# Kernel optimization log

Hardware: AMD Instinct MI355X
Metric: run time of the kernel (lower is better)

Reference implementation:

```python
import jax, jax.numpy as jnp
import numpy as np

D_MODEL = 1024
NUM_HEADS = 16
HEAD_DIM = D_MODEL // NUM_HEADS


def setup_inputs() -> dict:
    key = jax.random.key(0)
    ks = jax.random.split(key, 9)
    B, T = 2, 2048
    s = 1.0 / np.sqrt(D_MODEL)
    return {
        "x": jax.random.normal(ks[0], (B, T, D_MODEL), dtype=jnp.float32),
        "Wq": jax.random.normal(ks[1], (D_MODEL, D_MODEL), dtype=jnp.float32) * s,
        "bq": jnp.zeros((D_MODEL,), dtype=jnp.float32),
        "Wk": jax.random.normal(ks[2], (D_MODEL, D_MODEL), dtype=jnp.float32) * s,
        "bk": jnp.zeros((D_MODEL,), dtype=jnp.float32),
        "Wv": jax.random.normal(ks[3], (D_MODEL, D_MODEL), dtype=jnp.float32) * s,
        "bv": jnp.zeros((D_MODEL,), dtype=jnp.float32),
        "Wo": jax.random.normal(ks[4], (D_MODEL, D_MODEL), dtype=jnp.float32) * s,
        "bo": jnp.zeros((D_MODEL,), dtype=jnp.float32),
    }


def reference(x, Wq, bq, Wk, bk, Wv, bv, Wo, bo):
    B, T, D = x.shape
    H, Hd = NUM_HEADS, HEAD_DIM
    # Linear projections; weights stored as [in, out] (torch Linear transposed)
    q = (x @ Wq + bq).reshape(B, T, H, Hd)
    k = (x @ Wk + bk).reshape(B, T, H, Hd)
    v = (x @ Wv + bv).reshape(B, T, H, Hd)
    scale = 1.0 / jnp.sqrt(jnp.asarray(Hd, dtype=x.dtype))
    scores = jnp.einsum("bqhd,bkhd->bhqk", q, k) * scale  # [B,H,T,T]
    attn = jax.nn.softmax(scores, axis=-1)
    ctx = jnp.einsum("bhqk,bkhd->bqhd", attn, v).reshape(B, T, D)
    return ctx @ Wo + bo
```

## Files before the change

### kernel.cpp

```cpp
#include <hip/hip_runtime.h>


typedef unsigned short ushort_t;
typedef __attribute__((ext_vector_type(8))) short bf16x8;
typedef __attribute__((ext_vector_type(4))) short bf16x4;
typedef __attribute__((ext_vector_type(4))) float f32x4;

#define BATCH 2
#define SEQ   2048
#define DM    1024
#define NH    16
#define HD    64
#define MTOT  (BATCH*SEQ)

#if __has_builtin(__builtin_amdgcn_exp2f)
#define EXP2(x) __builtin_amdgcn_exp2f(x)
#else
#define EXP2(x) exp2f(x)
#endif

__device__ __forceinline__ ushort_t f2bf(float f) {
    union { float f; unsigned int u; } v; v.f = f;
    unsigned int r = v.u + 0x7fffu + ((v.u >> 16) & 1u);
    return (ushort_t)(r >> 16);
}

__device__ __forceinline__ void gload_lds16(const void* g, void* l) {
    __builtin_amdgcn_global_load_lds(
        (const __attribute__((address_space(1))) unsigned int*)g,
        (__attribute__((address_space(3))) unsigned int*)l, 16, 0, 0);
}

__global__ __launch_bounds__(256) void prep_kernel(const float* __restrict__ x,
                                                   const float* __restrict__ W0,
                                                   const float* __restrict__ W1,
                                                   const float* __restrict__ W2,
                                                   const float* __restrict__ W3,
                                                   ushort_t* __restrict__ xb,
                                                   ushort_t* __restrict__ Wtb) {
    __shared__ ushort_t tile[64][72];
    int bid = blockIdx.x, tid = threadIdx.x;
    if (bid < 4096) {
        int i = bid * 256 + tid;
        float4 v = ((const float4*)x)[i];
        ushort4 o;
        o.x = f2bf(v.x); o.y = f2bf(v.y); o.z = f2bf(v.z); o.w = f2bf(v.w);
        ((ushort4*)xb)[i] = o;
        return;
    }
    int b2 = bid - 4096;
    const float* Ws[4] = {W0, W1, W2, W3};
    const float* W = Ws[b2 >> 8];
    ushort_t* Wt = Wtb + (size_t)(b2 >> 8) * DM * DM;
    int k0 = ((b2 >> 4) & 15) * 64, n0 = (b2 & 15) * 64;
    int tr = tid >> 4;
    int tc = (tid & 15) * 4;
#pragma unroll
    for (int j = 0; j < 4; j++) {
        int r = j * 16 + tr;
        float4 v = *(const float4*)&W[(size_t)(k0 + r) * DM + n0 + tc];
        tile[r][tc + 0] = f2bf(v.x); tile[r][tc + 1] = f2bf(v.y);
        tile[r][tc + 2] = f2bf(v.z); tile[r][tc + 3] = f2bf(v.w);
    }
    __syncthreads();
#pragma unroll
    for (int j = 0; j < 4; j++) {
        int n = j * 16 + tr;
        ushort4 o;
        o.x = tile[tc + 0][n]; o.y = tile[tc + 1][n];
        o.z = tile[tc + 2][n]; o.w = tile[tc + 3][n];
        *(ushort4*)&Wt[(size_t)(n0 + n) * DM + k0 + tc] = o;
    }
}

__global__ __launch_bounds__(256) void gemm_qkv(const ushort_t* __restrict__ A,
                                                const ushort_t* __restrict__ Wtb,
                                                const float* __restrict__ bq,
                                                const float* __restrict__ bk,
                                                const float* __restrict__ bv,
                                                ushort_t* __restrict__ qo,
                                                ushort_t* __restrict__ ko,
                                                ushort_t* __restrict__ vo) {
    __shared__ ushort_t As[3][128 * 32];
    __shared__ ushort_t Bs[3][128 * 32];
    int sel = blockIdx.x >> 3;
    const ushort_t* Wt = Wtb + (size_t)sel * DM * DM;
    const float* bias = sel == 0 ? bq : (sel == 1 ? bk : bv);
    int tid = threadIdx.x;
    int w = tid >> 6, lane = tid & 63, lr = lane & 15, lg = lane >> 4;
    int wr = w >> 1, wc = w & 1;
    int m0 = blockIdx.y * 128, n0 = (blockIdx.x & 7) * 128;

    int srow = (w * 2) * 16 + (lane >> 2);
    int scb = (lane & 3) * 8;
    const ushort_t* ag = &A[(size_t)(m0 + srow) * DM + scb];
    const ushort_t* bg = &Wt[(size_t)(n0 + srow) * DM + scb];
    int ldst = (w * 2) * 1024;

    f32x4 acc[4][4] = {};

#pragma unroll
    for (int p = 0; p < 2; p++) {
        gload_lds16(ag + (size_t)p * 16 * DM, (char*)As[0] + ldst + p * 1024);
        gload_lds16(bg + (size_t)p * 16 * DM, (char*)Bs[0] + ldst + p * 1024);
    }

    int cur = 0;
    for (int kt = 0; kt < 32; ++kt) {
        if (kt + 1 < 32) {
            int nxt = cur + 1 == 3 ? 0 : cur + 1;
            int k0 = (kt + 1) << 5;
#pragma unroll
            for (int p = 0; p < 2; p++) {
                gload_lds16(ag + (size_t)p * 16 * DM + k0, (char*)As[nxt] + ldst + p * 1024);
                gload_lds16(bg + (size_t)p * 16 * DM + k0, (char*)Bs[nxt] + ldst + p * 1024);
            }
            __builtin_amdgcn_sched_barrier(0);
            asm volatile("s_waitcnt vmcnt(4)" ::: "memory");
        } else {
            __builtin_amdgcn_sched_barrier(0);
            asm volatile("s_waitcnt vmcnt(0)" ::: "memory");
        }
        __builtin_amdgcn_s_barrier();
        __builtin_amdgcn_sched_barrier(0);

        bf16x8 af[4], bfr[4];
#pragma unroll
        for (int i = 0; i < 4; i++) {
            af[i]  = *(const bf16x8*)&As[cur][(wr * 64 + i * 16 + lr) * 32 + lg * 8];
            bfr[i] = *(const bf16x8*)&Bs[cur][(wc * 64 + i * 16 + lr) * 32 + lg * 8];
        }
#pragma unroll
        for (int mi = 0; mi < 4; mi++)
#pragma unroll
            for (int ni = 0; ni < 4; ni++)
                acc[mi][ni] = __builtin_amdgcn_mfma_f32_16x16x32_bf16(
                    af[mi], bfr[ni], acc[mi][ni], 0, 0, 0);
        cur = cur + 1 == 3 ? 0 : cur + 1;
    }

    float scale = (sel == 0) ? 0.125f * 1.44269504f : 1.0f;
#pragma unroll
    for (int mi = 0; mi < 4; mi++) {
#pragma unroll
        for (int ni = 0; ni < 4; ni++) {
            f32x4 a = acc[mi][ni];
            int n = n0 + wc * 64 + ni * 16 + lr;
            float bs = bias[n];
            int mbase = m0 + wr * 64 + mi * 16 + lg * 4;
            int hh = n >> 6, d = n & 63;
            if (sel == 2) {
                int b = mbase >> 11, tt = mbase & 2047;
                size_t base = ((size_t)(b * NH + hh) * HD + d) * SEQ + tt;
                ushort4 pk;
                pk.x = f2bf(a[0] + bs); pk.y = f2bf(a[1] + bs);
                pk.z = f2bf(a[2] + bs); pk.w = f2bf(a[3] + bs);
                *(ushort4*)&vo[base] = pk;
            } else {
                ushort_t* o = sel ? ko : qo;
#pragma unroll
                for (int r = 0; r < 4; r++) {
                    int m = mbase + r;
                    int b = m >> 11, tt = m & 2047;
                    o[((size_t)(b * NH + hh) * SEQ + tt) * HD + d] =
                        f2bf((a[r] + bs) * scale);
                }
            }
        }
    }
}

__global__ __launch_bounds__(256) void gemm_out(const ushort_t* __restrict__ A,
                                                const ushort_t* __restrict__ Wt,
                                                const float* __restrict__ bias,
                                                float* __restrict__ out) {
    __shared__ ushort_t As[3][128 * 32];
    __shared__ ushort_t Bs[3][128 * 32];
    int tid = threadIdx.x;
    int w = tid >> 6, lane = tid & 63, lr = lane & 15, lg = lane >> 4;
    int wr = w >> 1, wc = w & 1;
    int m0 = blockIdx.y * 128, n0 = blockIdx.x * 128;

    int srow = (w * 2) * 16 + (lane >> 2);
    int scb = (lane & 3) * 8;
    const ushort_t* ag = &A[(size_t)(m0 + srow) * DM + scb];
    const ushort_t* bg = &Wt[(size_t)(n0 + srow) * DM + scb];
    int ldst = (w * 2) * 1024;

    f32x4 acc[4][4] = {};

#pragma unroll
    for (int p = 0; p < 2; p++) {
        gload_lds16(ag + (size_t)p * 16 * DM, (char*)As[0] + ldst + p * 1024);
        gload_lds16(bg + (size_t)p * 16 * DM, (char*)Bs[0] + ldst + p * 1024);
    }

    int cur = 0;
    for (int kt = 0; kt < 32; ++kt) {
        if (kt + 1 < 32) {
            int nxt = cur + 1 == 3 ? 0 : cur + 1;
            int k0 = (kt + 1) << 5;
#pragma unroll
            for (int p = 0; p < 2; p++) {
                gload_lds16(ag + (size_t)p * 16 * DM + k0, (char*)As[nxt] + ldst + p * 1024);
                gload_lds16(bg + (size_t)p * 16 * DM + k0, (char*)Bs[nxt] + ldst + p * 1024);
            }
            __builtin_amdgcn_sched_barrier(0);
            asm volatile("s_waitcnt vmcnt(4)" ::: "memory");
        } else {
            __builtin_amdgcn_sched_barrier(0);
            asm volatile("s_waitcnt vmcnt(0)" ::: "memory");
        }
        __builtin_amdgcn_s_barrier();
        __builtin_amdgcn_sched_barrier(0);

        bf16x8 af[4], bfr[4];
#pragma unroll
        for (int i = 0; i < 4; i++) {
            af[i]  = *(const bf16x8*)&As[cur][(wr * 64 + i * 16 + lr) * 32 + lg * 8];
            bfr[i] = *(const bf16x8*)&Bs[cur][(wc * 64 + i * 16 + lr) * 32 + lg * 8];
        }
#pragma unroll
        for (int mi = 0; mi < 4; mi++)
#pragma unroll
            for (int ni = 0; ni < 4; ni++)
                acc[mi][ni] = __builtin_amdgcn_mfma_f32_16x16x32_bf16(
                    af[mi], bfr[ni], acc[mi][ni], 0, 0, 0);
        cur = cur + 1 == 3 ? 0 : cur + 1;
    }

#pragma unroll
    for (int mi = 0; mi < 4; mi++) {
#pragma unroll
        for (int ni = 0; ni < 4; ni++) {
            f32x4 a = acc[mi][ni];
            int n = n0 + wc * 64 + ni * 16 + lr;
            float bs = bias[n];
            int mbase = m0 + wr * 64 + mi * 16 + lg * 4;
#pragma unroll
            for (int r = 0; r < 4; r++)
                out[(size_t)(mbase + r) * DM + n] = a[r] + bs;
        }
    }
}

__device__ __forceinline__ void softmax_pack(f32x4 (&s)[8], float& l_run,
                                             int4 (&pwv)[4]) {
    float rs0 = 0.f, rs1 = 0.f, rs2 = 0.f, rs3 = 0.f;
#pragma unroll
    for (int nt = 0; nt < 8; ++nt) {
        float p0 = EXP2(s[nt][0]);
        float p1 = EXP2(s[nt][1]);
        float p2 = EXP2(s[nt][2]);
        float p3 = EXP2(s[nt][3]);
        s[nt][0] = p0; s[nt][1] = p1; s[nt][2] = p2; s[nt][3] = p3;
        rs0 += p0; rs1 += p1; rs2 += p2; rs3 += p3;
    }
    float rs = (rs0 + rs1) + (rs2 + rs3);
    rs += __shfl_xor(rs, 16);
    rs += __shfl_xor(rs, 32);
    l_run += rs;
#pragma unroll
    for (int kk = 0; kk < 4; ++kk) {
        unsigned pw[4];
#pragma unroll
        for (int hh = 0; hh < 2; ++hh)
#pragma unroll
            for (int pr = 0; pr < 2; ++pr) {
                unsigned rr;
                asm("v_cvt_pk_bf16_f32 %0, %1, %2"
                    : "=v"(rr)
                    : "v"(s[kk + 4 * hh][2 * pr]), "v"(s[kk + 4 * hh][2 * pr + 1]));
                pw[hh * 2 + pr] = rr;
            }
        pwv[kk] = make_int4(pw[0], pw[1], pw[2], pw[3]);
    }
}

__global__ __launch_bounds__(512, 2) void attn_kernel(const ushort_t* __restrict__ Q,
                                                      const ushort_t* __restrict__ Kb,
                                                      const ushort_t* __restrict__ Vt,
                                                      ushort_t* __restrict__ Ctx) {
    __shared__ ushort_t Ks[2][128 * 64];
    __shared__ ushort_t Vs[2][64 * 128];

    int tid = threadIdx.x, w = tid >> 6, lane = tid & 63, lr = lane & 15, lg = lane >> 4;
    int orig = blockIdx.x;
    int wg = (orig & 7) * 32 + (orig >> 3);
    int qb = wg & 7, bh = wg >> 3;
    int q0 = qb * 256;

    const ushort_t* Qp = Q + (size_t)bh * SEQ * HD;
    const ushort_t* Kp = Kb + (size_t)bh * SEQ * HD;
    const ushort_t* Vp = Vt + (size_t)bh * HD * SEQ;

    int qrow = q0 + w * 16 + lr;
    bf16x8 aqA[2], aqB[2];
    aqA[0] = *(const bf16x8*)&Qp[(size_t)qrow * HD + lg * 8];
    aqA[1] = *(const bf16x8*)&Qp[(size_t)qrow * HD + 32 + lg * 8];
    aqB[0] = *(const bf16x8*)&Qp[(size_t)(qrow + 128) * HD + lg * 8];
    aqB[1] = *(const bf16x8*)&Qp[(size_t)(qrow + 128) * HD + 32 + lg * 8];

    f32x4 oaccA[4] = {}, oaccB[4] = {};
    float lA = 0.f, lB = 0.f;

    int krow = tid >> 3, kch = tid & 7;
    int kbyte = krow * 128 + ((kch * 16) ^ ((krow & 7) << 4));
    const ushort_t* kg0 = &Kp[(size_t)krow * HD + kch * 8];
    const ushort_t* kg1 = &Kp[(size_t)(krow + 64) * HD + kch * 8];
    int vrow = tid >> 4, vch = tid & 15;
    int S_a2 = (((vch >> 1) & 3) * 32 + (vch & 1) * 16 + (vch >> 3) * 4) * 2;
    int vswz = (vrow & 7) << 4;
    int vbyte0 = vrow * 256 + (S_a2 ^ vswz);
    int vbyte1 = vrow * 256 + ((S_a2 + 16) ^ vswz);
    const ushort_t* vg0 = &Vp[(size_t)vrow * SEQ + vch * 8];
    const ushort_t* vg1 = &Vp[(size_t)(vrow + 32) * SEQ + vch * 8];

    {
        bf16x8 k0v = *(const bf16x8*)kg0;
        bf16x8 k1v = *(const bf16x8*)kg1;
        bf16x8 v0v = *(const bf16x8*)vg0;
        bf16x8 v1v = *(const bf16x8*)vg1;
        *(bf16x8*)((char*)Ks[0] + kbyte) = k0v;
        *(bf16x8*)((char*)Ks[0] + kbyte + 64 * 128) = k1v;
        union { bf16x8 v; bf16x4 h[2]; } u0, u1;
        u0.v = v0v; u1.v = v1v;
        *(bf16x4*)((char*)Vs[0] + vbyte0) = u0.h[0];
        *(bf16x4*)((char*)Vs[0] + vbyte1) = u0.h[1];
        *(bf16x4*)((char*)Vs[0] + vbyte0 + 32 * 256) = u1.h[0];
        *(bf16x4*)((char*)Vs[0] + vbyte1 + 32 * 256) = u1.h[1];
    }
    __syncthreads();

    int kread = lr * 128;
    int kswz = (lr & 7) << 4;

    for (int t = 0; t < SEQ / 128; ++t) {
        int cur = t & 1;
        bf16x8 kr0, kr1, vr0, vr1;
        bool more = (t + 1 < SEQ / 128);
        if (more) {
            size_t ko_off = (size_t)(t + 1) * 128 * HD;
            int vo_off = (t + 1) * 128;
            kr0 = *(const bf16x8*)(kg0 + ko_off);
            kr1 = *(const bf16x8*)(kg1 + ko_off);
            vr0 = *(const bf16x8*)(vg0 + vo_off);
            vr1 = *(const bf16x8*)(vg1 + vo_off);
        }

        f32x4 sA[8], sB[8];
        __builtin_amdgcn_s_setprio(1);
#pragma unroll
        for (int nt = 0; nt < 8; ++nt) {
            f32x4 a = {}, b = {};
#pragma unroll
            for (int kk = 0; kk < 2; ++kk) {
                bf16x8 bk = *(const bf16x8*)((char*)Ks[cur] + nt * 2048 + kread +
                                             ((kk * 64 + lg * 16) ^ kswz));
                a = __builtin_amdgcn_mfma_f32_16x16x32_bf16(bk, aqA[kk], a, 0, 0, 0);
                b = __builtin_amdgcn_mfma_f32_16x16x32_bf16(bk, aqB[kk], b, 0, 0, 0);
            }
            sA[nt] = a; sB[nt] = b;
        }
        __builtin_amdgcn_s_setprio(0);

        int4 pwvA[4], pwvB[4];
        softmax_pack(sA, lA, pwvA);
        softmax_pack(sB, lB, pwvB);

        __builtin_amdgcn_s_setprio(1);
#pragma unroll
        for (int dt = 0; dt < 4; ++dt) {
            int vbase = (dt * 16 + lr) * 256;
#pragma unroll
            for (int kk = 0; kk < 4; ++kk) {
                bf16x8 bv = *(const bf16x8*)((char*)Vs[cur] + vbase +
                                             ((kk * 64 + lg * 16) ^ kswz));
                oaccA[dt] = __builtin_amdgcn_mfma_f32_16x16x32_bf16(
                    *(bf16x8*)&pwvA[kk], bv, oaccA[dt], 0, 0, 0);
                oaccB[dt] = __builtin_amdgcn_mfma_f32_16x16x32_bf16(
                    *(bf16x8*)&pwvB[kk], bv, oaccB[dt], 0, 0, 0);
            }
        }
        __builtin_amdgcn_s_setprio(0);

        if (more) {
            char* kd = (char*)Ks[cur ^ 1];
            char* vd = (char*)Vs[cur ^ 1];
            *(bf16x8*)(kd + kbyte) = kr0;
            *(bf16x8*)(kd + kbyte + 64 * 128) = kr1;
            union { bf16x8 v; bf16x4 h[2]; } u0, u1;
            u0.v = vr0; u1.v = vr1;
            *(bf16x4*)(vd + vbyte0) = u0.h[0];
            *(bf16x4*)(vd + vbyte1) = u0.h[1];
            *(bf16x4*)(vd + vbyte0 + 32 * 256) = u1.h[0];
            *(bf16x4*)(vd + vbyte1 + 32 * 256) = u1.h[1];
            __syncthreads();
        }
    }

    float invA = 1.0f / lA, invB = 1.0f / lB;
    float ivA[4], ivB[4];
#pragma unroll
    for (int r = 0; r < 4; ++r) {
        ivA[r] = __shfl(invA, lg * 4 + r);
        ivB[r] = __shfl(invB, lg * 4 + r);
    }
    int b = bh >> 4, h = bh & 15;
#pragma unroll
    for (int dt = 0; dt < 4; ++dt)
#pragma unroll
        for (int r = 0; r < 4; ++r) {
            int q = q0 + w * 16 + lg * 4 + r;
            Ctx[((size_t)(b * SEQ + q)) * DM + h * HD + dt * 16 + lr] =
                f2bf(oaccA[dt][r] * ivA[r]);
            Ctx[((size_t)(b * SEQ + q + 128)) * DM + h * HD + dt * 16 + lr] =
                f2bf(oaccB[dt][r] * ivB[r]);
        }
}

extern "C" void kernel_launch(void* const* d_in, const int* in_sizes, int n_in,
                              void* d_out, int out_size, void* d_ws, size_t ws_size,
                              hipStream_t stream) {
    const float* x  = (const float*)d_in[0];
    const float* Wq = (const float*)d_in[1];
    const float* bq = (const float*)d_in[2];
    const float* Wk = (const float*)d_in[3];
    const float* bk = (const float*)d_in[4];
    const float* Wv = (const float*)d_in[5];
    const float* bv = (const float*)d_in[6];
    const float* Wo = (const float*)d_in[7];
    const float* bo = (const float*)d_in[8];
    float* out = (float*)d_out;

    ushort_t* xbf = (ushort_t*)d_ws;
    ushort_t* wtb = xbf + (size_t)MTOT * DM;
    ushort_t* qbf = wtb + (size_t)4 * DM * DM;
    ushort_t* kbf = qbf + (size_t)MTOT * DM;
    ushort_t* vtb = kbf + (size_t)MTOT * DM;
    ushort_t* ctx = vtb + (size_t)MTOT * DM;

    prep_kernel<<<4096 + 1024, 256, 0, stream>>>(x, Wq, Wk, Wv, Wo, xbf, wtb);

    gemm_qkv<<<dim3(24, 32), 256, 0, stream>>>(xbf, wtb, bq, bk, bv, qbf, kbf, vtb);

    attn_kernel<<<256, 512, 0, stream>>>(qbf, kbf, vtb, ctx);

    gemm_out<<<dim3(8, 32), 256, 0, stream>>>(ctx, wtb + (size_t)3 * DM * DM, bo, out);
}
```

Measured before the change: 119.0 us.

## Split attention key range in two halves and merge partials in a combine kernel

New measurement: 127.5 us. +7.1%, slower.

```diff
diff --git a/kernel.cpp b/kernel.cpp
--- a/kernel.cpp
+++ b/kernel.cpp
@@ -23,6 +23,11 @@
     union { float f; unsigned int u; } v; v.f = f;
     unsigned int r = v.u + 0x7fffu + ((v.u >> 16) & 1u);
     return (ushort_t)(r >> 16);
+}
+
+__device__ __forceinline__ float bf2f(ushort_t u) {
+    union { unsigned int i; float f; } v; v.i = ((unsigned int)u) << 16;
+    return v.f;
 }
 
 __device__ __forceinline__ void gload_lds16(const void* g, void* l) {
@@ -280,15 +285,20 @@
 __global__ __launch_bounds__(512, 2) void attn_kernel(const ushort_t* __restrict__ Q,
                                                       const ushort_t* __restrict__ Kb,
                                                       const ushort_t* __restrict__ Vt,
-                                                      ushort_t* __restrict__ Ctx) {
+                                                      ushort_t* __restrict__ P0,
+                                                      ushort_t* __restrict__ P1,
+                                                      float* __restrict__ L0,
+                                                      float* __restrict__ L1) {
     __shared__ ushort_t Ks[2][128 * 64];
     __shared__ ushort_t Vs[2][64 * 128];
 
     int tid = threadIdx.x, w = tid >> 6, lane = tid & 63, lr = lane & 15, lg = lane >> 4;
     int orig = blockIdx.x;
-    int wg = (orig & 7) * 32 + (orig >> 3);
-    int qb = wg & 7, bh = wg >> 3;
+    int wg = (orig & 7) * 64 + (orig >> 3);
+    int bh = wg >> 4, rem = wg & 15;
+    int qb = rem >> 1, half = rem & 1;
     int q0 = qb * 256;
+    int t0 = half * 8;
 
     const ushort_t* Qp = Q + (size_t)bh * SEQ * HD;
     const ushort_t* Kp = Kb + (size_t)bh * SEQ * HD;
@@ -306,15 +316,15 @@
 
     int krow = tid >> 3, kch = tid & 7;
     int kbyte = krow * 128 + ((kch * 16) ^ ((krow & 7) << 4));
-    const ushort_t* kg0 = &Kp[(size_t)krow * HD + kch * 8];
-    const ushort_t* kg1 = &Kp[(size_t)(krow + 64) * HD + kch * 8];
+    const ushort_t* kg0 = &Kp[(size_t)(t0 * 128 + krow) * HD + kch * 8];
+    const ushort_t* kg1 = &Kp[(size_t)(t0 * 128 + krow + 64) * HD + kch * 8];
     int vrow = tid >> 4, vch = tid & 15;
     int S_a2 = (((vch >> 1) & 3) * 32 + (vch & 1) * 16 + (vch >> 3) * 4) * 2;
     int vswz = (vrow & 7) << 4;
     int vbyte0 = vrow * 256 + (S_a2 ^ vswz);
     int vbyte1 = vrow * 256 + ((S_a2 + 16) ^ vswz);
-    const ushort_t* vg0 = &Vp[(size_t)vrow * SEQ + vch * 8];
-    const ushort_t* vg1 = &Vp[(size_t)(vrow + 32) * SEQ + vch * 8];
+    const ushort_t* vg0 = &Vp[(size_t)vrow * SEQ + t0 * 128 + vch * 8];
+    const ushort_t* vg1 = &Vp[(size_t)(vrow + 32) * SEQ + t0 * 128 + vch * 8];
 
     {
         bf16x8 k0v = *(const bf16x8*)kg0;
@@ -335,10 +345,10 @@
     int kread = lr * 128;
     int kswz = (lr & 7) << 4;
 
-    for (int t = 0; t < SEQ / 128; ++t) {
+    for (int t = 0; t < 8; ++t) {
         int cur = t & 1;
         bf16x8 kr0, kr1, vr0, vr1;
-        bool more = (t + 1 < SEQ / 128);
+        bool more = (t + 1 < 8);
         if (more) {
             size_t ko_off = (size_t)(t + 1) * 128 * HD;
             int vo_off = (t + 1) * 128;
@@ -399,24 +409,44 @@
         }
     }
 
-    float invA = 1.0f / lA, invB = 1.0f / lB;
-    float ivA[4], ivB[4];
-#pragma unroll
-    for (int r = 0; r < 4; ++r) {
-        ivA[r] = __shfl(invA, lg * 4 + r);
-        ivB[r] = __shfl(invB, lg * 4 + r);
-    }
+    ushort_t* po = half ? P1 : P0;
+    float* lp = half ? L1 : L0;
     int b = bh >> 4, h = bh & 15;
 #pragma unroll
     for (int dt = 0; dt < 4; ++dt)
 #pragma unroll
         for (int r = 0; r < 4; ++r) {
             int q = q0 + w * 16 + lg * 4 + r;
-            Ctx[((size_t)(b * SEQ + q)) * DM + h * HD + dt * 16 + lr] =
-                f2bf(oaccA[dt][r] * ivA[r]);
-            Ctx[((size_t)(b * SEQ + q + 128)) * DM + h * HD + dt * 16 + lr] =
-                f2bf(oaccB[dt][r] * ivB[r]);
-        }
+            po[((size_t)(b * SEQ + q)) * DM + h * HD + dt * 16 + lr] =
+                f2bf(oaccA[dt][r]);
+            po[((size_t)(b * SEQ + q + 128)) * DM + h * HD + dt * 16 + lr] =
+                f2bf(oaccB[dt][r]);
+        }
+    if (lg == 0) {
+        lp[(bh << 11) + q0 + w * 16 + lr] = lA;
+        lp[(bh << 11) + q0 + w * 16 + lr + 128] = lB;
+    }
+}
+
+__global__ __launch_bounds__(256) void combine_kernel(const ushort_t* __restrict__ P0,
+                                                      const ushort_t* __restrict__ P1,
+                                                      const float* __restrict__ L0,
+                                                      const float* __restrict__ L1,
+                                                      ushort_t* __restrict__ Ctx) {
+    int i = blockIdx.x * 256 + threadIdx.x;
+    int m = i >> 8, c = i & 255;
+    int n0 = c * 4, h = n0 >> 6;
+    int b = m >> 11, q = m & 2047;
+    int li = ((b * NH + h) << 11) + q;
+    float inv = 1.0f / (L0[li] + L1[li]);
+    ushort4 a = *(const ushort4*)&P0[(size_t)m * DM + n0];
+    ushort4 bb = *(const ushort4*)&P1[(size_t)m * DM + n0];
+    ushort4 o;
+    o.x = f2bf((bf2f(a.x) + bf2f(bb.x)) * inv);
+    o.y = f2bf((bf2f(a.y) + bf2f(bb.y)) * inv);
+    o.z = f2bf((bf2f(a.z) + bf2f(bb.z)) * inv);
+    o.w = f2bf((bf2f(a.w) + bf2f(bb.w)) * inv);
+    *(ushort4*)&Ctx[(size_t)m * DM + n0] = o;
 }
 
 extern "C" void kernel_launch(void* const* d_in, const int* in_sizes, int n_in,
@@ -439,12 +469,17 @@
     ushort_t* kbf = qbf + (size_t)MTOT * DM;
     ushort_t* vtb = kbf + (size_t)MTOT * DM;
     ushort_t* ctx = vtb + (size_t)MTOT * DM;
+    float* l0 = (float*)wtb;
+    float* l1 = (float*)(wtb + (size_t)512 * 1024);
+    ushort_t* part1 = xbf;
 
     prep_kernel<<<4096 + 1024, 256, 0, stream>>>(x, Wq, Wk, Wv, Wo, xbf, wtb);
 
     gemm_qkv<<<dim3(24, 32), 256, 0, stream>>>(xbf, wtb, bq, bk, bv, qbf, kbf, vtb);
 
-    attn_kernel<<<256, 512, 0, stream>>>(qbf, kbf, vtb, ctx);
+    attn_kernel<<<512, 512, 0, stream>>>(qbf, kbf, vtb, ctx, part1, l0, l1);
+
+    combine_kernel<<<4096, 256, 0, stream>>>(ctx, part1, l0, l1, ctx);
 
     gemm_out<<<dim3(8, 32), 256, 0, stream>>>(ctx, wtb + (size_t)3 * DM * DM, bo, out);
 }
```
